# Performance work log

Measured on AMD Instinct MI355X. Metric: run time of the kernel, lower is better.

Reference implementation:

```python
import jax, jax.numpy as jnp
import numpy as np

K_MASK = -2.3819763e+38
NUM_HEADS = 16
NUM_KV_HEADS = 8
HEAD_DIM = 128
FEATURES = 2048
QUERY_SCALE = 0.08838834764831845  # head_dim ** -0.5
ROPE_BASE = 10000
SOFT_CAP = 50.0
WINDOW = 1024


def apply_rope(inputs, positions, base_frequency=ROPE_BASE):
    # inputs: [B, L, N, H], positions: [B, L]
    head_dim = inputs.shape[-1]
    fraction = 2.0 * jnp.arange(0, head_dim // 2, dtype=jnp.float32) / head_dim
    timescale = jnp.asarray(base_frequency, jnp.float32) ** fraction
    sinusoid = positions[..., None].astype(jnp.float32) / timescale[None, None, :]
    sinusoid = sinusoid[..., None, :]  # [B, L, 1, H/2]
    sin, cos = jnp.sin(sinusoid), jnp.cos(sinusoid)
    first, second = jnp.split(inputs, 2, axis=-1)
    out = jnp.concatenate([first * cos - second * sin,
                           second * cos + first * sin], axis=-1)
    return out.astype(inputs.dtype)


def setup_inputs() -> dict:
    key = jax.random.key(0)
    ks = jax.random.split(key, 4)
    B, T, D = 2, 2048, FEATURES
    x = jax.random.normal(ks[0], (B, T, D), dtype=jnp.float32)
    segment_pos = jnp.broadcast_to(jnp.arange(T, dtype=jnp.int32)[None, :], (B, T))
    # causal prefill mask [B, T, S] with S == T
    attn_mask = jnp.broadcast_to(
        jnp.tril(jnp.ones((T, T), dtype=bool))[None], (B, T, T))
    wq = jax.random.normal(ks[1], (NUM_HEADS, D, HEAD_DIM), dtype=jnp.float32) * 0.02
    wkv = jax.random.normal(ks[2], (2, NUM_KV_HEADS, D, HEAD_DIM), dtype=jnp.float32) * 0.02
    wo = jax.random.normal(ks[3], (NUM_HEADS, HEAD_DIM, D), dtype=jnp.float32) * 0.02
    return {"x": x, "segment_pos": segment_pos, "attn_mask": attn_mask,
            "wq": wq, "wkv": wkv, "wo": wo}


def reference(x, segment_pos, attn_mask, wq, wkv, wo):
    # Projections
    q = jnp.einsum('BTD,NDH->BTNH', x, wq)              # [B,T,N,H]
    kv = jnp.einsum('BSD,CKDH->CBSKH', x, wkv)          # [2,B,S,K,H]
    k, v = kv[0], kv[1]

    # RoPE + query scaling
    q = apply_rope(q, segment_pos) * QUERY_SCALE
    k = apply_rope(k, segment_pos)

    # GQA: fold query heads into (K groups, G heads per group)
    B, T, N, H = q.shape
    K, G = NUM_KV_HEADS, N // NUM_KV_HEADS
    qg = q.reshape(B, T, K, G, H)
    logits = jnp.einsum('BTKGH,BSKH->BTKGS', qg, k).reshape(B, T, N, -1)

    # Logit soft-capping
    logits = jnp.tanh(logits / SOFT_CAP) * SOFT_CAP

    # Sliding-window mask (prefill: end_index=0, cache_len = S)
    S = attn_mask.shape[-1]
    cache_positions = jnp.arange(S)[None, None, :]       # [1,1,S]
    sp = segment_pos[:, :, None]                         # [B,T,1]
    sliding = (cache_positions > sp - WINDOW) & (cache_positions < sp + WINDOW)
    mask = jnp.logical_and(attn_mask, sliding)

    padded = jnp.where(mask[:, :, None, :], logits, K_MASK)
    probs = jax.nn.softmax(padded, axis=-1).astype(k.dtype)

    pg = probs.reshape(B, T, K, G, S)
    encoded = jnp.einsum('BTKGS,BSKH->BTKGH', pg, v).reshape(B, T, N, H)
    return jnp.einsum('BTNH,NHD->BTD', encoded, wo)
```

## Files before the change

kernel.cpp:

```cpp
#include <hip/hip_runtime.h>

typedef __attribute__((ext_vector_type(8))) short short8;
typedef __attribute__((ext_vector_type(4))) float f32x4;
typedef __attribute__((ext_vector_type(4))) float f4;
typedef __attribute__((ext_vector_type(4))) unsigned short u16x4;

#define MFMA_B16 __builtin_amdgcn_mfma_f32_16x16x32_bf16

__device__ __forceinline__ unsigned short f2bf(float f) {
    union { float f; unsigned int u; } v; v.f = f;
    unsigned int r = v.u + 0x7fffu + ((v.u >> 16) & 1u);
    return (unsigned short)(r >> 16);
}
__device__ __forceinline__ float bf2f(unsigned short h) {
    union { unsigned int u; float f; } v; v.u = ((unsigned int)h) << 16;
    return v.f;
}
__device__ __forceinline__ float fexp2(float x) {
    float r; asm("v_exp_f32 %0, %1" : "=v"(r) : "v"(x)); return r;
}
__device__ __forceinline__ unsigned int cvt_pk_bf16(float lo, float hi) {
    unsigned int r;
    asm("v_cvt_pk_bf16_f32 %0, %1, %2" : "=v"(r) : "v"(lo), "v"(hi));
    return r;
}
__device__ __forceinline__ void gload_lds16(const void* g, void* l) {
    __builtin_amdgcn_global_load_lds(
        (const __attribute__((address_space(1))) unsigned int*)g,
        (__attribute__((address_space(3))) unsigned int*)l, 16, 0, 0);
}

__global__ void conv_all(const float* __restrict__ x, unsigned short* __restrict__ xb,
                         const float* __restrict__ wq, const float* __restrict__ wkv,
                         unsigned short* __restrict__ wt_qkv,
                         const float* __restrict__ wo, unsigned short* __restrict__ wt_o) {
    __shared__ float tile[64 * 65];
    const int bx = blockIdx.x, tid = threadIdx.x;
    if (bx < 8192) {
        int i = bx * 256 + tid;
        f4 v = ((const f4*)x)[i];
        u16x4 o;
        o[0] = f2bf(v[0]); o[1] = f2bf(v[1]); o[2] = f2bf(v[2]); o[3] = f2bf(v[3]);
        ((u16x4*)xb)[i] = o;
        return;
    }
    if (bx < 10240) {
        const int flat = bx - 8192;
        const int d0 = (flat & 31) * 64, f0 = (flat >> 5) * 64;
        const int head = f0 >> 7;
        const int h0 = f0 & 127;
        const float* src;
        float scl;
        if (head < 16)      { src = wq + (size_t)head * 2048 * 128;         scl = 0.08838834764831845f; }
        else if (head < 24) { src = wkv + (size_t)(head - 16) * 2048 * 128; scl = 0.057707801635558534f; }
        else                { src = wkv + (size_t)(head - 16) * 2048 * 128; scl = 1.f; }
        {
            int hh = tid & 63, dq = tid >> 6;
            #pragma unroll
            for (int r = 0; r < 16; ++r) {
                int dd = r * 4 + dq;
                tile[dd * 65 + hh] = src[(size_t)(d0 + dd) * 128 + h0 + hh] * scl;
            }
        }
        __syncthreads();
        {
            int dd = tid & 63, fq = tid >> 6;
            #pragma unroll
            for (int r = 0; r < 16; ++r) {
                int fl = r * 4 + fq;
                wt_qkv[(size_t)(f0 + fl) * 2048 + d0 + dd] = f2bf(tile[dd * 65 + fl]);
            }
        }
        return;
    }
    {
        const int flat = bx - 10240;
        const int d0 = (flat & 31) * 64, r0 = (flat >> 5) * 64;
        int cc = tid & 63, rq = tid >> 6;
        #pragma unroll
        for (int r = 0; r < 16; ++r) {
            int rr = r * 4 + rq;
            tile[rr * 65 + cc] = wo[(size_t)(r0 + rr) * 2048 + d0 + cc];
        }
        __syncthreads();
        #pragma unroll
        for (int r = 0; r < 16; ++r) {
            int rr = r * 4 + rq;
            wt_o[(size_t)(d0 + rr) * 2048 + r0 + cc] = f2bf(tile[cc * 65 + rr]);
        }
    }
}


__global__ __launch_bounds__(512, 2)
void gemm8p(const unsigned short* __restrict__ A,
            const unsigned short* __restrict__ Bt,
            unsigned short* __restrict__ C,
            int ldk, int ldc, int nt, int ksplit, size_t cstride) {
    __shared__ __align__(16) unsigned short LDS[65536];
    const int tid = threadIdx.x, lane = tid & 63, w = tid >> 6;
    const int wr = w >> 2, wc = w & 3;
    const int l15 = lane & 15, l4 = lane >> 4;
    int nwg = gridDim.x * gridDim.y;
    int wg = blockIdx.y * gridDim.x + blockIdx.x;
    int swz = (wg & 7) * (nwg >> 3) + (wg >> 3);
    int bx = swz % gridDim.x, by = swz / gridDim.x;
    int slice = 0;
    if (ksplit) { slice = by & 1; by >>= 1; }
    unsigned short* Cs = C + (size_t)slice * cstride;
    const int brow = by * 256, bcol = bx * 256;
    const size_t koff = (size_t)slice * nt * 64;
    const int wg_a = w & 3;
    const int wg_b = wr;
    const int rA = wg_a * 8 + (lane >> 3);
    const int rB = wg_b * 8 + (lane >> 3);
    const int cgS = ((lane & 7) ^ (lane >> 3)) * 8;
    const unsigned short* aP = A + (size_t)(brow + wr * 128 + rA) * ldk + koff + cgS;
    const unsigned short* bP = Bt + (size_t)(bcol + wc * 64 + rB) * ldk + koff + cgS;
    const int ldsA0 = wr * 8192 + (wg_a * 64 + lane) * 8;
    const int ldsB0 = wc * 4096 + (wg_b * 64 + lane) * 8;
    const int aRd = (wr * 128 + l15) * 64;
    const int bRd = (wc * 64 + l15) * 64;
    const int c0 = ((0 + l4) ^ (l15 & 7)) * 8;
    const int c1 = ((4 + l4) ^ (l15 & 7)) * 8;
    f32x4 acc[8][4] = {};
    gload_lds16(aP,                    &LDS[ldsA0]);
    gload_lds16(bP,                    &LDS[16384 + ldsB0]);
    gload_lds16(aP + (size_t)32 * ldk, &LDS[ldsA0 + 2048]);
    gload_lds16(bP + (size_t)16 * ldk, &LDS[16384 + ldsB0 + 1024]);
    gload_lds16(bP + (size_t)32 * ldk, &LDS[16384 + ldsB0 + 2048]);
    gload_lds16(bP + (size_t)48 * ldk, &LDS[16384 + ldsB0 + 3072]);
    gload_lds16(aP + (size_t)64 * ldk, &LDS[ldsA0 + 4096]);
    gload_lds16(aP + (size_t)96 * ldk, &LDS[ldsA0 + 6144]);
    {
        const unsigned short* a1 = aP + 64;
        const unsigned short* b1 = bP + 64;
        gload_lds16(a1,                    &LDS[32768 + ldsA0]);
        gload_lds16(b1,                    &LDS[49152 + ldsB0]);
        gload_lds16(a1 + (size_t)32 * ldk, &LDS[32768 + ldsA0 + 2048]);
        gload_lds16(b1 + (size_t)16 * ldk, &LDS[49152 + ldsB0 + 1024]);
        gload_lds16(b1 + (size_t)32 * ldk, &LDS[49152 + ldsB0 + 2048]);
        gload_lds16(b1 + (size_t)48 * ldk, &LDS[49152 + ldsB0 + 3072]);
    }
    asm volatile("s_waitcnt vmcnt(6)" ::: "memory");
    __builtin_amdgcn_s_barrier();
    __builtin_amdgcn_sched_barrier(0);

    short8 af[4][2], bl[2][2], bh[2][2];
    for (int t = 0; t < nt - 1; ++t) {
        const int bufA = (t & 1) << 15, bufB = bufA + 16384;
        const int sA = ((t + 1) & 1) << 15;
        const bool pf2 = (t + 2) < nt;
        const unsigned short* ap1 = aP + (size_t)(t + 1) * 64;
        const unsigned short* ap2 = aP + (size_t)(t + 2) * 64;
        const unsigned short* bp2 = bP + (size_t)(t + 2) * 64;
        #pragma unroll
        for (int m = 0; m < 4; ++m) {
            af[m][0] = *(const short8*)&LDS[bufA + aRd + m * 1024 + c0];
            af[m][1] = *(const short8*)&LDS[bufA + aRd + m * 1024 + c1];
        }
        #pragma unroll
        for (int n = 0; n < 2; ++n) {
            bl[n][0] = *(const short8*)&LDS[bufB + bRd + n * 1024 + c0];
            bl[n][1] = *(const short8*)&LDS[bufB + bRd + n * 1024 + c1];
        }
        gload_lds16(ap1 + (size_t)64 * ldk, &LDS[sA + ldsA0 + 4096]);
        gload_lds16(ap1 + (size_t)96 * ldk, &LDS[sA + ldsA0 + 6144]);
        __builtin_amdgcn_s_barrier();
        __builtin_amdgcn_sched_barrier(0);
        __builtin_amdgcn_s_setprio(1);
        #pragma unroll
        for (int kk = 0; kk < 2; ++kk)
            #pragma unroll
            for (int m = 0; m < 4; ++m)
                #pragma unroll
                for (int n = 0; n < 2; ++n)
                    acc[m][n] = MFMA_B16(af[m][kk], bl[n][kk], acc[m][n], 0, 0, 0);
        __builtin_amdgcn_s_setprio(0);
        asm volatile("s_waitcnt vmcnt(6)" ::: "memory");
        __builtin_amdgcn_s_barrier();
        __builtin_amdgcn_sched_barrier(0);
        #pragma unroll
        for (int n = 0; n < 2; ++n) {
            bh[n][0] = *(const short8*)&LDS[bufB + bRd + (n + 2) * 1024 + c0];
            bh[n][1] = *(const short8*)&LDS[bufB + bRd + (n + 2) * 1024 + c1];
        }
        if (pf2) { gload_lds16(ap2, &LDS[bufA + ldsA0]);
                   gload_lds16(bp2, &LDS[bufB + ldsB0]); }
        __builtin_amdgcn_s_barrier();
        __builtin_amdgcn_sched_barrier(0);
        __builtin_amdgcn_s_setprio(1);
        #pragma unroll
        for (int kk = 0; kk < 2; ++kk)
            #pragma unroll
            for (int m = 0; m < 4; ++m)
                #pragma unroll
                for (int n = 0; n < 2; ++n)
                    acc[m][n + 2] = MFMA_B16(af[m][kk], bh[n][kk], acc[m][n + 2], 0, 0, 0);
        __builtin_amdgcn_s_setprio(0);
        asm volatile("s_waitcnt vmcnt(6)" ::: "memory");
        __builtin_amdgcn_s_barrier();
        __builtin_amdgcn_sched_barrier(0);
        #pragma unroll
        for (int m = 0; m < 4; ++m) {
            af[m][0] = *(const short8*)&LDS[bufA + aRd + (m + 4) * 1024 + c0];
            af[m][1] = *(const short8*)&LDS[bufA + aRd + (m + 4) * 1024 + c1];
        }
        if (pf2) { gload_lds16(ap2 + (size_t)32 * ldk, &LDS[bufA + ldsA0 + 2048]);
                   gload_lds16(bp2 + (size_t)16 * ldk, &LDS[bufB + ldsB0 + 1024]); }
        __builtin_amdgcn_s_barrier();
        __builtin_amdgcn_sched_barrier(0);
        __builtin_amdgcn_s_setprio(1);
        #pragma unroll
        for (int kk = 0; kk < 2; ++kk)
            #pragma unroll
            for (int m = 0; m < 4; ++m)
                #pragma unroll
                for (int n = 0; n < 2; ++n)
                    acc[m + 4][n] = MFMA_B16(af[m][kk], bl[n][kk], acc[m + 4][n], 0, 0, 0);
        __builtin_amdgcn_s_setprio(0);
        asm volatile("s_waitcnt vmcnt(6)" ::: "memory");
        __builtin_amdgcn_s_barrier();
        __builtin_amdgcn_sched_barrier(0);
        if (pf2) { gload_lds16(bp2 + (size_t)32 * ldk, &LDS[bufB + ldsB0 + 2048]);
                   gload_lds16(bp2 + (size_t)48 * ldk, &LDS[bufB + ldsB0 + 3072]); }
        __builtin_amdgcn_s_barrier();
        __builtin_amdgcn_sched_barrier(0);
        __builtin_amdgcn_s_setprio(1);
        #pragma unroll
        for (int kk = 0; kk < 2; ++kk)
            #pragma unroll
            for (int m = 0; m < 4; ++m)
                #pragma unroll
                for (int n = 0; n < 2; ++n)
                    acc[m + 4][n + 2] = MFMA_B16(af[m][kk], bh[n][kk], acc[m + 4][n + 2], 0, 0, 0);
        __builtin_amdgcn_s_setprio(0);
        asm volatile("s_waitcnt vmcnt(6)" ::: "memory");
        __builtin_amdgcn_s_barrier();
        __builtin_amdgcn_sched_barrier(0);
    }
    asm volatile("s_waitcnt vmcnt(0)" ::: "memory");
    __builtin_amdgcn_s_barrier();
    {
        const int bufA = ((nt - 1) & 1) << 15, bufB = bufA + 16384;
        #pragma unroll
        for (int m = 0; m < 4; ++m) {
            af[m][0] = *(const short8*)&LDS[bufA + aRd + m * 1024 + c0];
            af[m][1] = *(const short8*)&LDS[bufA + aRd + m * 1024 + c1];
        }
        #pragma unroll
        for (int n = 0; n < 2; ++n) {
            bl[n][0] = *(const short8*)&LDS[bufB + bRd + n * 1024 + c0];
            bl[n][1] = *(const short8*)&LDS[bufB + bRd + n * 1024 + c1];
            bh[n][0] = *(const short8*)&LDS[bufB + bRd + (n + 2) * 1024 + c0];
            bh[n][1] = *(const short8*)&LDS[bufB + bRd + (n + 2) * 1024 + c1];
        }
        #pragma unroll
        for (int kk = 0; kk < 2; ++kk)
            #pragma unroll
            for (int m = 0; m < 4; ++m)
                #pragma unroll
                for (int n = 0; n < 2; ++n) {
                    acc[m][n]     = MFMA_B16(af[m][kk], bl[n][kk], acc[m][n], 0, 0, 0);
                    acc[m][n + 2] = MFMA_B16(af[m][kk], bh[n][kk], acc[m][n + 2], 0, 0, 0);
                }
        #pragma unroll
        for (int m = 0; m < 4; ++m) {
            af[m][0] = *(const short8*)&LDS[bufA + aRd + (m + 4) * 1024 + c0];
            af[m][1] = *(const short8*)&LDS[bufA + aRd + (m + 4) * 1024 + c1];
        }
        #pragma unroll
        for (int kk = 0; kk < 2; ++kk)
            #pragma unroll
            for (int m = 0; m < 4; ++m)
                #pragma unroll
                for (int n = 0; n < 2; ++n) {
                    acc[m + 4][n]     = MFMA_B16(af[m][kk], bl[n][kk], acc[m + 4][n], 0, 0, 0);
                    acc[m + 4][n + 2] = MFMA_B16(af[m][kk], bh[n][kk], acc[m + 4][n + 2], 0, 0, 0);
                }
    }
    #pragma unroll
    for (int m = 0; m < 8; ++m)
        #pragma unroll
        for (int n = 0; n < 4; ++n)
            #pragma unroll
            for (int j = 0; j < 4; ++j) {
                int row = brow + wr * 128 + m * 16 + l4 * 4 + j;
                int col = bcol + wc * 64 + n * 16 + l15;
                Cs[(size_t)row * ldc + col] = f2bf(acc[m][n][j]);
            }
}

__global__ void addparts(const unsigned short* __restrict__ p0,
                         const unsigned short* __restrict__ p1,
                         float* __restrict__ out) {
    int i = blockIdx.x * 256 + threadIdx.x;
    short8 a = ((const short8*)p0)[i];
    short8 b = ((const short8*)p1)[i];
    f4 lo, hi;
    #pragma unroll
    for (int j = 0; j < 4; ++j)
        lo[j] = bf2f((unsigned short)a[j]) + bf2f((unsigned short)b[j]);
    #pragma unroll
    for (int j = 0; j < 4; ++j)
        hi[j] = bf2f((unsigned short)a[j + 4]) + bf2f((unsigned short)b[j + 4]);
    ((f4*)out)[2 * i] = lo;
    ((f4*)out)[2 * i + 1] = hi;
}

__global__ void rope_vt(const unsigned short* __restrict__ qkv,
                        const int* __restrict__ segpos,
                        unsigned short* __restrict__ q_r,
                        unsigned short* __restrict__ k_r,
                        unsigned short* __restrict__ v_t) {
    __shared__ unsigned short tile[64][72];
    const int bx = blockIdx.x, tid = threadIdx.x;
    if (bx < 49152) {
        const int bt = bx & 4095;
        const int hd = (bx >> 12) * 2 + (tid >> 7);
        const int b = bt >> 11, t = bt & 2047;
        const int h = tid & 127;
        const unsigned short* in = (hd < 16)
            ? qkv + (size_t)bt * 4096 + hd * 128
            : qkv + (size_t)bt * 4096 + 2048 + (hd - 16) * 128;
        int pos = segpos[bt];
        int i = h & 63;
        float inv_ts = __expf((float)i * (-9.210340371976184f / 64.f));
        float ang = (float)pos * inv_ts;
        float s = __sinf(ang), c = __cosf(ang);
        float x1 = bf2f(in[i]);
        float x2 = bf2f(in[i + 64]);
        float o = (h < 64) ? (x1 * c - x2 * s) : (x2 * c + x1 * s);
        if (hd < 16) {
            q_r[((size_t)((b * 16 + hd) * 2048 + t)) * 128 + h] = f2bf(o);
        } else {
            int kh = hd - 16;
            k_r[((size_t)((b * 8 + kh) * 2048 + t)) * 128 + h] = f2bf(o);
        }
        return;
    }
    {
        const int flat = bx - 49152;
        const int tt0 = (flat & 31) * 64;
        const int y = (flat >> 5) & 15;
        const int b = flat >> 9;
        const int kh = y >> 1, hb = (y & 1) * 64;
        int c = tid & 63, rq = tid >> 6;
        #pragma unroll
        for (int r = 0; r < 16; ++r) {
            int tt = r * 4 + rq;
            tile[tt][c] = qkv[(size_t)(b * 2048 + tt0 + tt) * 4096 + 3072 + kh * 128 + hb + c];
        }
        __syncthreads();
        #pragma unroll
        for (int r = 0; r < 16; ++r) {
            int hr = r * 4 + rq;
            v_t[((size_t)(b * 8 + kh) * 128 + hb + hr) * 2048 + tt0 + c] = tile[c][hr];
        }
    }
}


__device__ __forceinline__ void stage_kv(const unsigned short* kbase, const unsigned short* vbase,
                                         unsigned short* Ksb, unsigned short* Vtb,
                                         int st, int tid) {
    #pragma unroll
    for (int r = 0; r < 2; ++r) {
        int e = (r * 512 + tid) * 8;
        int krow = e >> 7, kcol = e & 127;
        gload_lds16(kbase + (size_t)(st * 64 + krow) * 128 + (kcol ^ ((krow & 7) << 3)), Ksb + e);
        int vrow = e >> 6, vcol = e & 63;
        gload_lds16(vbase + (size_t)vrow * 2048 + st * 64 + (vcol ^ ((vrow & 7) << 3)), Vtb + e);
    }
}

__global__ __launch_bounds__(512, 4)
void attn_kernel(const unsigned short* __restrict__ q_r,
                 const unsigned short* __restrict__ k_r,
                 const unsigned short* __restrict__ v_t,
                 unsigned short* __restrict__ enc) {
    __shared__ __align__(16) unsigned short Ks[2][64 * 128];
    __shared__ __align__(16) unsigned short Vt[2][128 * 64];
    __shared__ __align__(16) unsigned short Pl[8][16 * 64];
    const int tid = threadIdx.x, lane = tid & 63, wave = tid >> 6;
    const int l15 = lane & 15, l4 = lane >> 4;
    const int flat = blockIdx.x;
    const int xcd = flat & 7, g = flat >> 3;
    const int pair = xcd * 2 + (g >> 5);
    const int qb = (g & 32) ? (g & 31) : 31 - (g & 31);
    const int kh = pair >> 1, b = pair & 1;
    const int n = kh * 2 + (wave >> 2);
    const int wq = wave & 3;
    short8 qf[4];
    {
        const unsigned short* qp =
            q_r + ((size_t)((b * 16 + n) * 2048 + qb * 64 + wq * 16 + l15)) * 128 + l4 * 8;
        #pragma unroll
        for (int kk = 0; kk < 4; ++kk) qf[kk] = *(const short8*)(qp + kk * 32);
    }
    short8 ones;
    #pragma unroll
    for (int e = 0; e < 8; ++e) ones[e] = (short)0x3F80;
    f32x4 Of[8] = {};
    f32x4 accl = {};
    int t_lo = qb * 64 - 1023; if (t_lo < 0) t_lo = 0;
    const int st0 = t_lo >> 6;
    const unsigned short* kbase = k_r + (size_t)(b * 8 + kh) * 2048 * 128;
    const unsigned short* vbase = v_t + (size_t)(b * 8 + kh) * 128 * 2048;

    stage_kv(kbase, vbase, Ks[0], Vt[0], st0, tid);
    __syncthreads();
    int cur = 0;
    for (int st = st0; st <= qb; ++st) {
        if (st < qb)
            stage_kv(kbase, vbase, Ks[cur ^ 1], Vt[cur ^ 1], st + 1, tid);
        f32x4 sf[4] = {};
        __builtin_amdgcn_s_setprio(1);
        #pragma unroll
        for (int nc = 0; nc < 4; ++nc) {
            int row = nc * 16 + l15;
            int sw = (l15 & 7) << 3;
            #pragma unroll
            for (int kk = 0; kk < 4; ++kk) {
                short8 bfr = *(const short8*)&Ks[cur][row * 128 + ((kk * 32 + l4 * 8) ^ sw)];
                sf[nc] = MFMA_B16(qf[kk], bfr, sf[nc], 0, 0, 0);
            }
        }
        __builtin_amdgcn_s_setprio(0);
        const int mode = (st == qb) ? 1 : ((qb >= 16 && st == st0) ? 2 : 0);
        #pragma unroll
        for (int j = 0; j < 4; ++j) {
            int trow = qb * 64 + wq * 16 + l4 * 4 + j;
            int prow = l4 * 4 + j;
            int psw = (prow & 7) << 3;
            float pp[4];
            #pragma unroll
            for (int nc = 0; nc < 4; ++nc) {
                float ex = fexp2(sf[nc][j]);
                float p = fexp2(-144.26950408889634f * __builtin_amdgcn_rcpf(ex + 1.f));
                if (mode) {
                    int s = st * 64 + nc * 16 + l15;
                    bool ok = (mode == 1) ? (s <= trow) : (s >= trow - 1023);
                    p = ok ? p : 0.f;
                }
                pp[nc] = p;
            }
            unsigned int k01 = cvt_pk_bf16(pp[0], pp[1]);
            unsigned int k23 = cvt_pk_bf16(pp[2], pp[3]);
            unsigned short* Pr = &Pl[wave][prow * 64];
            Pr[l15 ^ psw]        = (unsigned short)k01;
            Pr[(16 + l15) ^ psw] = (unsigned short)(k01 >> 16);
            Pr[(32 + l15) ^ psw] = (unsigned short)k23;
            Pr[(48 + l15) ^ psw] = (unsigned short)(k23 >> 16);
        }
        {
            int asw = (l15 & 7) << 3;
            __builtin_amdgcn_s_setprio(1);
            #pragma unroll
            for (int ks = 0; ks < 2; ++ks) {
                short8 af = *(const short8*)&Pl[wave][l15 * 64 + ((ks * 32 + l4 * 8) ^ asw)];
                accl = MFMA_B16(af, ones, accl, 0, 0, 0);
                #pragma unroll
                for (int hc = 0; hc < 8; ++hc) {
                    int vrow = hc * 16 + l15;
                    short8 bfr = *(const short8*)&Vt[cur][vrow * 64 + ((ks * 32 + l4 * 8) ^ asw)];
                    Of[hc] = MFMA_B16(af, bfr, Of[hc], 0, 0, 0);
                }
            }
            __builtin_amdgcn_s_setprio(0);
        }
        __syncthreads();
        cur ^= 1;
    }
    f32x4 inv;
    #pragma unroll
    for (int j = 0; j < 4; ++j) inv[j] = 1.f / accl[j];
    #pragma unroll
    for (int hc = 0; hc < 8; ++hc)
        #pragma unroll
        for (int j = 0; j < 4; ++j) {
            size_t row = (size_t)(b * 2048 + qb * 64 + wq * 16 + l4 * 4 + j);
            enc[row * 2048 + n * 128 + hc * 16 + l15] = f2bf(Of[hc][j] * inv[j]);
        }
}


extern "C" void kernel_launch(void* const* d_in, const int* in_sizes, int n_in,
                              void* d_out, int out_size, void* d_ws, size_t ws_size,
                              hipStream_t stream) {
    const float* x   = (const float*)d_in[0];
    const int* segp  = (const int*)d_in[1];
    const float* wq  = (const float*)d_in[3];
    const float* wkv = (const float*)d_in[4];
    const float* wo  = (const float*)d_in[5];
    float* out = (float*)d_out;
    char* ws = (char*)d_ws;
    if (ws_size < ((size_t)104 << 20)) return;

    unsigned short* xb    = (unsigned short*)(ws);
    unsigned short* wqkvt = (unsigned short*)(ws + ((size_t)16 << 20));
    unsigned short* qkv   = (unsigned short*)(ws + ((size_t)32 << 20));
    unsigned short* q_r   = (unsigned short*)(ws + ((size_t)64 << 20));
    unsigned short* k_r   = (unsigned short*)(ws + ((size_t)80 << 20));
    unsigned short* v_t   = (unsigned short*)(ws + ((size_t)88 << 20));
    unsigned short* wo_t  = (unsigned short*)(ws + ((size_t)96 << 20));
    unsigned short* enc   = (unsigned short*)(ws + ((size_t)32 << 20));
    unsigned short* part  = (unsigned short*)(ws + ((size_t)64 << 20));

    conv_all<<<11264, 256, 0, stream>>>(x, xb, wq, wkv, wqkvt, wo, wo_t);
    gemm8p<<<dim3(16, 16), 512, 0, stream>>>(xb, wqkvt, qkv, 2048, 4096, 32, 0, 0);
    rope_vt<<<50176, 256, 0, stream>>>(qkv, segp, q_r, k_r, v_t);
    attn_kernel<<<512, 512, 0, stream>>>(q_r, k_r, v_t, enc);
    gemm8p<<<dim3(8, 32), 512, 0, stream>>>(enc, wo_t, part, 2048, 2048, 16, 1, (size_t)4096 * 2048);
    addparts<<<4096, 256, 0, stream>>>(part, part + (size_t)4096 * 2048, out);
}
```

Before: 205.2 us.

## Halve attention KV tile to 32 keys and share P buffers between wave pairs

```diff
diff --git a/kernel.cpp b/kernel.cpp
--- a/kernel.cpp
+++ b/kernel.cpp
@@ -361,17 +361,14 @@
 }
 
 
-__device__ __forceinline__ void stage_kv(const unsigned short* kbase, const unsigned short* vbase,
-                                         unsigned short* Ksb, unsigned short* Vtb,
-                                         int st, int tid) {
-    #pragma unroll
-    for (int r = 0; r < 2; ++r) {
-        int e = (r * 512 + tid) * 8;
-        int krow = e >> 7, kcol = e & 127;
-        gload_lds16(kbase + (size_t)(st * 64 + krow) * 128 + (kcol ^ ((krow & 7) << 3)), Ksb + e);
-        int vrow = e >> 6, vcol = e & 63;
-        gload_lds16(vbase + (size_t)vrow * 2048 + st * 64 + (vcol ^ ((vrow & 7) << 3)), Vtb + e);
-    }
+__device__ __forceinline__ void stage_kv32(const unsigned short* kbase, const unsigned short* vbase,
+                                           unsigned short* Ksb, unsigned short* Vtb,
+                                           int st, int tid) {
+    int e = tid * 8;
+    int krow = tid >> 4, kcol = e & 127;
+    gload_lds16(kbase + (size_t)(st * 32 + krow) * 128 + (kcol ^ ((krow & 7) << 3)), Ksb + e);
+    int vrow = tid >> 2, vg = tid & 3;
+    gload_lds16(vbase + (size_t)vrow * 2048 + st * 32 + ((vg ^ ((vrow >> 1) & 3)) * 8), Vtb + e);
 }
 
 __global__ __launch_bounds__(512, 4)
@@ -379,9 +376,9 @@
                  const unsigned short* __restrict__ k_r,
                  const unsigned short* __restrict__ v_t,
                  unsigned short* __restrict__ enc) {
-    __shared__ __align__(16) unsigned short Ks[2][64 * 128];
-    __shared__ __align__(16) unsigned short Vt[2][128 * 64];
-    __shared__ __align__(16) unsigned short Pl[8][16 * 64];
+    __shared__ __align__(16) unsigned short Ks[2][32 * 128];
+    __shared__ __align__(16) unsigned short Vt[2][128 * 32];
+    __shared__ __align__(16) unsigned short Pl[4][16 * 64];
     const int tid = threadIdx.x, lane = tid & 63, wave = tid >> 6;
     const int l15 = lane & 15, l4 = lane >> 4;
     const int flat = blockIdx.x;
@@ -391,6 +388,8 @@
     const int kh = pair >> 1, b = pair & 1;
     const int n = kh * 2 + (wave >> 2);
     const int wq = wave & 3;
+    const int colbase = (wave & 1) * 32;
+    unsigned short* Plb = Pl[wave >> 1];
     short8 qf[4];
     {
         const unsigned short* qp =
@@ -404,20 +403,21 @@
     f32x4 Of[8] = {};
     f32x4 accl = {};
     int t_lo = qb * 64 - 1023; if (t_lo < 0) t_lo = 0;
-    const int st0 = t_lo >> 6;
+    const int st0 = t_lo >> 5;
+    const int stL = qb * 2 + 1;
     const unsigned short* kbase = k_r + (size_t)(b * 8 + kh) * 2048 * 128;
     const unsigned short* vbase = v_t + (size_t)(b * 8 + kh) * 128 * 2048;
 
-    stage_kv(kbase, vbase, Ks[0], Vt[0], st0, tid);
+    stage_kv32(kbase, vbase, Ks[0], Vt[0], st0, tid);
     __syncthreads();
     int cur = 0;
-    for (int st = st0; st <= qb; ++st) {
-        if (st < qb)
-            stage_kv(kbase, vbase, Ks[cur ^ 1], Vt[cur ^ 1], st + 1, tid);
-        f32x4 sf[4] = {};
+    for (int st = st0; st <= stL; ++st) {
+        if (st < stL)
+            stage_kv32(kbase, vbase, Ks[cur ^ 1], Vt[cur ^ 1], st + 1, tid);
+        f32x4 sf[2] = {};
         __builtin_amdgcn_s_setprio(1);
         #pragma unroll
-        for (int nc = 0; nc < 4; ++nc) {
+        for (int nc = 0; nc < 2; ++nc) {
             int row = nc * 16 + l15;
             int sw = (l15 & 7) << 3;
             #pragma unroll
@@ -427,45 +427,41 @@
             }
         }
         __builtin_amdgcn_s_setprio(0);
-        const int mode = (st == qb) ? 1 : ((qb >= 16 && st == st0) ? 2 : 0);
+        const int mode = ((st >= 2 * qb) ? 1 : 0) | ((qb >= 16 && st <= st0 + 1) ? 2 : 0);
         #pragma unroll
         for (int j = 0; j < 4; ++j) {
             int trow = qb * 64 + wq * 16 + l4 * 4 + j;
             int prow = l4 * 4 + j;
             int psw = (prow & 7) << 3;
-            float pp[4];
-            #pragma unroll
-            for (int nc = 0; nc < 4; ++nc) {
+            float pp[2];
+            #pragma unroll
+            for (int nc = 0; nc < 2; ++nc) {
                 float ex = fexp2(sf[nc][j]);
                 float p = fexp2(-144.26950408889634f * __builtin_amdgcn_rcpf(ex + 1.f));
                 if (mode) {
-                    int s = st * 64 + nc * 16 + l15;
-                    bool ok = (mode == 1) ? (s <= trow) : (s >= trow - 1023);
+                    int s = st * 32 + nc * 16 + l15;
+                    bool ok = true;
+                    if (mode & 1) ok = ok && (s <= trow);
+                    if (mode & 2) ok = ok && (s >= trow - 1023);
                     p = ok ? p : 0.f;
                 }
                 pp[nc] = p;
             }
             unsigned int k01 = cvt_pk_bf16(pp[0], pp[1]);
-            unsigned int k23 = cvt_pk_bf16(pp[2], pp[3]);
-            unsigned short* Pr = &Pl[wave][prow * 64];
-            Pr[l15 ^ psw]        = (unsigned short)k01;
-            Pr[(16 + l15) ^ psw] = (unsigned short)(k01 >> 16);
-            Pr[(32 + l15) ^ psw] = (unsigned short)k23;
-            Pr[(48 + l15) ^ psw] = (unsigned short)(k23 >> 16);
+            unsigned short* Pr = &Plb[prow * 64];
+            Pr[(colbase + l15) ^ psw]      = (unsigned short)k01;
+            Pr[(colbase + 16 + l15) ^ psw] = (unsigned short)(k01 >> 16);
         }
         {
             int asw = (l15 & 7) << 3;
             __builtin_amdgcn_s_setprio(1);
-            #pragma unroll
-            for (int ks = 0; ks < 2; ++ks) {
-                short8 af = *(const short8*)&Pl[wave][l15 * 64 + ((ks * 32 + l4 * 8) ^ asw)];
-                accl = MFMA_B16(af, ones, accl, 0, 0, 0);
-                #pragma unroll
-                for (int hc = 0; hc < 8; ++hc) {
-                    int vrow = hc * 16 + l15;
-                    short8 bfr = *(const short8*)&Vt[cur][vrow * 64 + ((ks * 32 + l4 * 8) ^ asw)];
-                    Of[hc] = MFMA_B16(af, bfr, Of[hc], 0, 0, 0);
-                }
+            short8 af = *(const short8*)&Plb[l15 * 64 + ((colbase + l4 * 8) ^ asw)];
+            accl = MFMA_B16(af, ones, accl, 0, 0, 0);
+            #pragma unroll
+            for (int hc = 0; hc < 8; ++hc) {
+                int vrow = hc * 16 + l15;
+                short8 bfr = *(const short8*)&Vt[cur][vrow * 32 + ((l4 ^ ((vrow >> 1) & 3)) * 8)];
+                Of[hc] = MFMA_B16(af, bfr, Of[hc], 0, 0, 0);
             }
             __builtin_amdgcn_s_setprio(0);
         }
```

New measurement: 206.4 us. Within noise of the previous version (+0.6%).
